# Optimization experiments

Hardware: AMD Instinct MI355X
Metric: run time of the kernel (lower is better)

Reference implementation:

```python
import jax, jax.numpy as jnp
import numpy as np

NUM_CLASSES = 100000
EMBED_DIM = 512
BATCH = 16384
ALPHA = 0.95  # center update momentum: diff = (1 - ALPHA) * (centers - features)


def setup_inputs() -> dict:
    key = jax.random.key(0)
    k1, k2, k3 = jax.random.split(key, 3)
    features = jax.random.normal(k1, (BATCH, EMBED_DIM), dtype=jnp.float32)
    labels = jax.random.randint(k2, (BATCH,), 0, NUM_CLASSES, dtype=jnp.int64)
    center_var = jax.random.normal(k3, (NUM_CLASSES, EMBED_DIM), dtype=jnp.float32)
    return {"features": features, "labels": labels, "center_var": center_var}


def reference(features, labels, center_var):
    # gather per-label centers: [B, D]
    labels = labels.reshape(-1)
    centers_batch = center_var[labels]
    # update delta, 0.05 * (center - feature)
    diff = (1.0 - ALPHA) * (centers_batch - features)
    # scatter-subtract with duplicate-label accumulation (tf scatter_nd_sub semantics)
    new_centers = center_var.at[labels].add(-diff)
    # MSE between features and their (pre-update) centers
    loss = jnp.mean(jnp.square(features - centers_batch))
    return loss, new_centers
```

## Files before the change

kernel.cpp:

```cpp
#include <hip/hip_runtime.h>

constexpr int NUM_CLASSES  = 100000;
constexpr int EMBED_DIM    = 512;
constexpr int BATCH        = 16384;
constexpr int CENTER_ELEMS = NUM_CLASSES * EMBED_DIM;
constexpr int NSLOTS       = 256;
constexpr int KMAX         = 8;
constexpr float UPDATE_SCALE = 0.05f;
constexpr float INV_COUNT  = 1.0f / 8388608.0f;

typedef float f4 __attribute__((ext_vector_type(4)));

constexpr size_t WS_COUNTS_OFF  = 0;
constexpr size_t WS_ITEMS_OFF   = WS_COUNTS_OFF + (size_t)NUM_CLASSES;
constexpr size_t WS_TOUCHED_OFF = WS_ITEMS_OFF + (size_t)NUM_CLASSES * KMAX;
constexpr size_t WS_NTOUCH_OFF  = WS_TOUCHED_OFF + (size_t)BATCH;
constexpr size_t WS_PART_OFF    = WS_NTOUCH_OFF + 16;
constexpr size_t WS_NEW         = (WS_PART_OFF + NSLOTS) * 4;

__global__ void zero_ws_kernel(int* __restrict__ counts,
                               int* __restrict__ ntouched,
                               float* __restrict__ partials) {
    int g = blockIdx.x * blockDim.x + threadIdx.x;
    if (g < NUM_CLASSES) counts[g] = 0;
    if (g == 0) *ntouched = 0;
    if (g < NSLOTS) partials[g] = 0.0f;
}

__global__ void hist_kernel(const int* __restrict__ labels,
                            int* __restrict__ counts,
                            int* __restrict__ items,
                            int* __restrict__ touched,
                            int* __restrict__ ntouched) {
    int b = blockIdx.x * blockDim.x + threadIdx.x;
    if (b < BATCH) {
        int l = labels[b];
        int r = atomicAdd(&counts[l], 1);
        if (r < KMAX) items[l * KMAX + r] = b;
        if (r == 0) {
            int s = atomicAdd(ntouched, 1);
            touched[s] = l;
        }
    }
}

__global__ __launch_bounds__(256) void copy_shift_kernel(
        const float* __restrict__ src,
        float* __restrict__ out) {
    constexpr int NF4 = CENTER_ELEMS / 4;
    const int gid    = blockIdx.x * blockDim.x + threadIdx.x;
    const int stride = gridDim.x * blockDim.x;
    int j = gid;
    if (gid == 0) {
        out[1] = src[0];
        out[2] = src[1];
        out[3] = src[2];
        out[CENTER_ELEMS] = src[CENTER_ELEMS - 1];
        j = stride;
    }
    for (; j < NF4; j += stride) {
        const float* p = src + 4 * j - 1;
        f4 v;
        v.x = p[0];
        v.y = p[1];
        v.z = p[2];
        v.w = p[3];
        __builtin_nontemporal_store(v, (f4*)out + j);
    }
}

__global__ __launch_bounds__(128) void touched_update_kernel(
        const float* __restrict__ features,
        const int*   __restrict__ labels,
        const float* __restrict__ centers,
        const int*   __restrict__ counts,
        const int*   __restrict__ items,
        const int*   __restrict__ touched,
        const int*   __restrict__ ntouched,
        float* __restrict__ out,
        float* __restrict__ partials) {
    const int nb = *ntouched;
    if (blockIdx.x >= nb) return;
    const int c   = touched[blockIdx.x];
    const int cnt = counts[c];
    const int t   = threadIdx.x;

    const f4 c4 = ((const f4*)(centers + (size_t)c * EMBED_DIM))[t];
    f4 s; s.x = 0.f; s.y = 0.f; s.z = 0.f; s.w = 0.f;
    float local = 0.0f;

    if (cnt <= KMAX) {
        for (int i = 0; i < cnt; ++i) {
            const int b = items[c * KMAX + i];
            const f4 f = ((const f4*)(features + (size_t)b * EMBED_DIM))[t];
            float dx = f.x - c4.x, dy = f.y - c4.y, dz = f.z - c4.z, dw = f.w - c4.w;
            s.x += dx; s.y += dy; s.z += dz; s.w += dw;
            local += dx * dx + dy * dy + dz * dz + dw * dw;
        }
    } else {
        for (int b = 0; b < BATCH; ++b) {
            if (labels[b] == c) {
                const f4 f = ((const f4*)(features + (size_t)b * EMBED_DIM))[t];
                float dx = f.x - c4.x, dy = f.y - c4.y, dz = f.z - c4.z, dw = f.w - c4.w;
                s.x += dx; s.y += dy; s.z += dz; s.w += dw;
                local += dx * dx + dy * dy + dz * dz + dw * dw;
            }
        }
    }

    f4 n4;
    n4.x = fmaf(UPDATE_SCALE, s.x, c4.x);
    n4.y = fmaf(UPDATE_SCALE, s.y, c4.y);
    n4.z = fmaf(UPDATE_SCALE, s.z, c4.z);
    n4.w = fmaf(UPDATE_SCALE, s.w, c4.w);

    #pragma unroll
    for (int off = 32; off > 0; off >>= 1)
        local += __shfl_down(local, off, 64);
    if ((t & 63) == 0)
        atomicAdd(&partials[(blockIdx.x * 2 + (t >> 6)) & (NSLOTS - 1)], local);

    __shared__ float row[EMBED_DIM];
    ((f4*)row)[t] = n4;
    __syncthreads();

    const size_t R = (size_t)c * EMBED_DIM;
    if (t < 127) {
        f4 o;
        o.x = row[4 * t + 3];
        o.y = row[4 * t + 4];
        o.z = row[4 * t + 5];
        o.w = row[4 * t + 6];
        ((f4*)(out + R + 4))[t] = o;
    } else {
        out[R + 1] = row[0];
        out[R + 2] = row[1];
        out[R + 3] = row[2];
        out[R + EMBED_DIM] = row[EMBED_DIM - 1];
    }
}

__global__ __launch_bounds__(64) void finalize_loss_kernel(
        const float* __restrict__ partials,
        float* __restrict__ out) {
    float v = 0.0f;
    #pragma unroll
    for (int k = 0; k < NSLOTS / 64; ++k)
        v += partials[threadIdx.x + k * 64];
    #pragma unroll
    for (int off = 32; off > 0; off >>= 1)
        v += __shfl_down(v, off, 64);
    if (threadIdx.x == 0)
        out[0] = v * INV_COUNT;
}


__global__ void copy_centers_kernel(const float* __restrict__ src,
                                    float* __restrict__ dst,
                                    float* __restrict__ ws_partials) {
    int gid = blockIdx.x * blockDim.x + threadIdx.x;
    if (gid < NSLOTS) ws_partials[gid] = 0.0f;
    int stride = gridDim.x * blockDim.x;
    for (int i = gid; i < CENTER_ELEMS; i += stride) dst[i] = src[i];
}

__global__ __launch_bounds__(128) void update_kernel(
        const float* __restrict__ features,
        const int*   __restrict__ labels,
        const float* __restrict__ centers,
        float* __restrict__ out,
        float* __restrict__ ws_partials) {
    const int b = blockIdx.x;
    const int label = labels[b];
    const int t = threadIdx.x;
    const float4 f = ((const float4*)(features + (size_t)b * EMBED_DIM))[t];
    const float4 c = ((const float4*)(centers + (size_t)label * EMBED_DIM))[t];
    float4 d;
    d.x = f.x - c.x; d.y = f.y - c.y; d.z = f.z - c.z; d.w = f.w - c.w;
    float* nrow = out + 1 + (size_t)label * EMBED_DIM + (size_t)t * 4;
    atomicAdd(nrow + 0, UPDATE_SCALE * d.x);
    atomicAdd(nrow + 1, UPDATE_SCALE * d.y);
    atomicAdd(nrow + 2, UPDATE_SCALE * d.z);
    atomicAdd(nrow + 3, UPDATE_SCALE * d.w);
    float local = d.x * d.x + d.y * d.y + d.z * d.z + d.w * d.w;
    #pragma unroll
    for (int off = 32; off > 0; off >>= 1)
        local += __shfl_down(local, off, 64);
    if ((t & 63) == 0)
        atomicAdd(&ws_partials[(b * 2 + (t >> 6)) & (NSLOTS - 1)], local);
}


extern "C" void kernel_launch(void* const* d_in, const int* in_sizes, int n_in,
                              void* d_out, int out_size, void* d_ws, size_t ws_size,
                              hipStream_t stream) {
    const float* features = (const float*)d_in[0];
    const int*   labels   = (const int*)d_in[1];
    const float* centers  = (const float*)d_in[2];
    float* out = (float*)d_out;

    if (ws_size >= WS_NEW) {
        int* wsi       = (int*)d_ws;
        int* counts    = wsi + WS_COUNTS_OFF;
        int* items     = wsi + WS_ITEMS_OFF;
        int* touched   = wsi + WS_TOUCHED_OFF;
        int* ntouched  = wsi + WS_NTOUCH_OFF;
        float* partials = (float*)(wsi + WS_PART_OFF);

        zero_ws_kernel<<<(NUM_CLASSES + 255) / 256, 256, 0, stream>>>(
            counts, ntouched, partials);
        hist_kernel<<<(BATCH + 255) / 256, 256, 0, stream>>>(
            labels, counts, items, touched, ntouched);
        copy_shift_kernel<<<2048, 256, 0, stream>>>(centers, out);
        touched_update_kernel<<<BATCH, 128, 0, stream>>>(
            features, labels, centers, counts, items, touched, ntouched,
            out, partials);
        finalize_loss_kernel<<<1, 64, 0, stream>>>(partials, out);
    } else {
        float* partials = (float*)d_ws;
        copy_centers_kernel<<<8192, 256, 0, stream>>>(centers, out + 1, partials);
        update_kernel<<<BATCH, 128, 0, stream>>>(features, labels, centers, out, partials);
        finalize_loss_kernel<<<1, 64, 0, stream>>>(partials, out);
    }
}
```

Baseline: 426.7 us.

## Use aligned vector loads with lane shuffles in copy-shift and pack two classes per block

The shifted copy of the centers now does one aligned 16-byte load per element group and gets the preceding element from the neighbouring lane by a wave shuffle. Only lane 0 of each wave does an extra scalar load. Previously it did four unaligned scalar loads. The nontemporal store is replaced by a normal vector store. The touched-class update kernel now handles two classes per 256-thread block, which halves the number of blocks launched and the number of early-exit blocks.

```diff
diff --git a/kernel.cpp b/kernel.cpp
--- a/kernel.cpp
+++ b/kernel.cpp
@@ -50,26 +50,25 @@
     constexpr int NF4 = CENTER_ELEMS / 4;
     const int gid    = blockIdx.x * blockDim.x + threadIdx.x;
     const int stride = gridDim.x * blockDim.x;
-    int j = gid;
-    if (gid == 0) {
-        out[1] = src[0];
-        out[2] = src[1];
-        out[3] = src[2];
-        out[CENTER_ELEMS] = src[CENTER_ELEMS - 1];
-        j = stride;
-    }
-    for (; j < NF4; j += stride) {
-        const float* p = src + 4 * j - 1;
-        f4 v;
-        v.x = p[0];
-        v.y = p[1];
-        v.z = p[2];
-        v.w = p[3];
-        __builtin_nontemporal_store(v, (f4*)out + j);
-    }
-}
-
-__global__ __launch_bounds__(128) void touched_update_kernel(
+    const int lane   = threadIdx.x & 63;
+    for (int j = gid; j < NF4; j += stride) {
+        f4 v = ((const f4*)src)[j];
+        float wprev = __shfl_up(v.w, 1, 64);
+        if (lane == 0 && j > 0) wprev = src[4 * j - 1];
+        if (j == 0) {
+            out[1] = v.x;
+            out[2] = v.y;
+            out[3] = v.z;
+            out[CENTER_ELEMS] = src[CENTER_ELEMS - 1];
+        } else {
+            f4 o;
+            o.x = wprev; o.y = v.x; o.z = v.y; o.w = v.z;
+            ((f4*)out)[j] = o;
+        }
+    }
+}
+
+__global__ __launch_bounds__(256) void touched_update_kernel(
         const float* __restrict__ features,
         const int*   __restrict__ labels,
         const float* __restrict__ centers,
@@ -79,64 +78,76 @@
         const int*   __restrict__ ntouched,
         float* __restrict__ out,
         float* __restrict__ partials) {
-    const int nb = *ntouched;
-    if (blockIdx.x >= nb) return;
-    const int c   = touched[blockIdx.x];
-    const int cnt = counts[c];
-    const int t   = threadIdx.x;
-
-    const f4 c4 = ((const f4*)(centers + (size_t)c * EMBED_DIM))[t];
-    f4 s; s.x = 0.f; s.y = 0.f; s.z = 0.f; s.w = 0.f;
-    float local = 0.0f;
-
-    if (cnt <= KMAX) {
-        for (int i = 0; i < cnt; ++i) {
-            const int b = items[c * KMAX + i];
-            const f4 f = ((const f4*)(features + (size_t)b * EMBED_DIM))[t];
-            float dx = f.x - c4.x, dy = f.y - c4.y, dz = f.z - c4.z, dw = f.w - c4.w;
-            s.x += dx; s.y += dy; s.z += dz; s.w += dw;
-            local += dx * dx + dy * dy + dz * dz + dw * dw;
-        }
-    } else {
-        for (int b = 0; b < BATCH; ++b) {
-            if (labels[b] == c) {
-                const f4 f = ((const f4*)(features + (size_t)b * EMBED_DIM))[t];
-                float dx = f.x - c4.x, dy = f.y - c4.y, dz = f.z - c4.z, dw = f.w - c4.w;
+    const int nb   = *ntouched;
+    const int t    = threadIdx.x;
+    const int half = t >> 7;
+    const int ts   = t & 127;
+    const int idx  = blockIdx.x * 2 + half;
+    const bool active = idx < nb;
+
+    __shared__ float row[2][EMBED_DIM];
+    int c = 0;
+
+    if (active) {
+        c = touched[idx];
+        const int cnt = counts[c];
+
+        const f4 c4 = ((const f4*)(centers + (size_t)c * EMBED_DIM))[ts];
+        f4 s; s.x = 0.f; s.y = 0.f; s.z = 0.f; s.w = 0.f;
+        float local = 0.0f;
+
+        if (cnt <= KMAX) {
+            for (int i = 0; i < cnt; ++i) {
+                const int b = items[c * KMAX + i];
+                const f4 f = ((const f4*)(features + (size_t)b * EMBED_DIM))[ts];
+                float dx = f.x - c4.x, dy = f.y - c4.y;
+                float dz = f.z - c4.z, dw = f.w - c4.w;
                 s.x += dx; s.y += dy; s.z += dz; s.w += dw;
                 local += dx * dx + dy * dy + dz * dz + dw * dw;
             }
-        }
-    }
-
-    f4 n4;
-    n4.x = fmaf(UPDATE_SCALE, s.x, c4.x);
-    n4.y = fmaf(UPDATE_SCALE, s.y, c4.y);
-    n4.z = fmaf(UPDATE_SCALE, s.z, c4.z);
-    n4.w = fmaf(UPDATE_SCALE, s.w, c4.w);
-
-    #pragma unroll
-    for (int off = 32; off > 0; off >>= 1)
-        local += __shfl_down(local, off, 64);
-    if ((t & 63) == 0)
-        atomicAdd(&partials[(blockIdx.x * 2 + (t >> 6)) & (NSLOTS - 1)], local);
-
-    __shared__ float row[EMBED_DIM];
-    ((f4*)row)[t] = n4;
+        } else {
+            for (int b = 0; b < BATCH; ++b) {
+                if (labels[b] == c) {
+                    const f4 f = ((const f4*)(features + (size_t)b * EMBED_DIM))[ts];
+                    float dx = f.x - c4.x, dy = f.y - c4.y;
+                    float dz = f.z - c4.z, dw = f.w - c4.w;
+                    s.x += dx; s.y += dy; s.z += dz; s.w += dw;
+                    local += dx * dx + dy * dy + dz * dz + dw * dw;
+                }
+            }
+        }
+
+        f4 n4;
+        n4.x = fmaf(UPDATE_SCALE, s.x, c4.x);
+        n4.y = fmaf(UPDATE_SCALE, s.y, c4.y);
+        n4.z = fmaf(UPDATE_SCALE, s.z, c4.z);
+        n4.w = fmaf(UPDATE_SCALE, s.w, c4.w);
+
+        #pragma unroll
+        for (int off = 32; off > 0; off >>= 1)
+            local += __shfl_down(local, off, 64);
+        if ((t & 63) == 0)
+            atomicAdd(&partials[(idx * 2 + (ts >> 6)) & (NSLOTS - 1)], local);
+
+        ((f4*)row[half])[ts] = n4;
+    }
     __syncthreads();
 
-    const size_t R = (size_t)c * EMBED_DIM;
-    if (t < 127) {
-        f4 o;
-        o.x = row[4 * t + 3];
-        o.y = row[4 * t + 4];
-        o.z = row[4 * t + 5];
-        o.w = row[4 * t + 6];
-        ((f4*)(out + R + 4))[t] = o;
-    } else {
-        out[R + 1] = row[0];
-        out[R + 2] = row[1];
-        out[R + 3] = row[2];
-        out[R + EMBED_DIM] = row[EMBED_DIM - 1];
+    if (active) {
+        const size_t R = (size_t)c * EMBED_DIM;
+        if (ts < 127) {
+            f4 o;
+            o.x = row[half][4 * ts + 3];
+            o.y = row[half][4 * ts + 4];
+            o.z = row[half][4 * ts + 5];
+            o.w = row[half][4 * ts + 6];
+            ((f4*)(out + R + 4))[ts] = o;
+        } else {
+            out[R + 1] = row[half][0];
+            out[R + 2] = row[half][1];
+            out[R + 3] = row[half][2];
+            out[R + EMBED_DIM] = row[half][EMBED_DIM - 1];
+        }
     }
 }
 
@@ -212,7 +223,7 @@
         hist_kernel<<<(BATCH + 255) / 256, 256, 0, stream>>>(
             labels, counts, items, touched, ntouched);
         copy_shift_kernel<<<2048, 256, 0, stream>>>(centers, out);
-        touched_update_kernel<<<BATCH, 128, 0, stream>>>(
+        touched_update_kernel<<<(BATCH + 1) / 2, 256, 0, stream>>>(
             features, labels, centers, counts, items, touched, ntouched,
             out, partials);
         finalize_loss_kernel<<<1, 64, 0, stream>>>(partials, out);
```

Result: faster. 407.8 us (-4.4%).

## Fuse center copy and touched-row update into one wave-per-row streaming kernel

Applied to the files above, without the earlier changes.

Replaces the separate shifted copy of all centers and the per-touched-class update kernel with one kernel where each wavefront walks class rows. Each wave reads its center row once, applies the accumulated feature deltas if the class has labels, and writes the shifted output row using a lane shuffle instead of shared memory. This removes the second pass that rewrote touched rows and drops the touched-list bookkeeping and its atomics. The cost is per-row branching and a per-class count lookup in the streaming loop, and some lanes go idle where touched rows are unevenly spread.

```diff
diff --git a/kernel.cpp b/kernel.cpp
--- a/kernel.cpp
+++ b/kernel.cpp
@@ -13,130 +13,114 @@
 
 constexpr size_t WS_COUNTS_OFF  = 0;
 constexpr size_t WS_ITEMS_OFF   = WS_COUNTS_OFF + (size_t)NUM_CLASSES;
-constexpr size_t WS_TOUCHED_OFF = WS_ITEMS_OFF + (size_t)NUM_CLASSES * KMAX;
-constexpr size_t WS_NTOUCH_OFF  = WS_TOUCHED_OFF + (size_t)BATCH;
-constexpr size_t WS_PART_OFF    = WS_NTOUCH_OFF + 16;
+constexpr size_t WS_PART_OFF    = WS_ITEMS_OFF + (size_t)NUM_CLASSES * KMAX;
 constexpr size_t WS_NEW         = (WS_PART_OFF + NSLOTS) * 4;
 
 __global__ void zero_ws_kernel(int* __restrict__ counts,
-                               int* __restrict__ ntouched,
                                float* __restrict__ partials) {
     int g = blockIdx.x * blockDim.x + threadIdx.x;
     if (g < NUM_CLASSES) counts[g] = 0;
-    if (g == 0) *ntouched = 0;
     if (g < NSLOTS) partials[g] = 0.0f;
 }
 
 __global__ void hist_kernel(const int* __restrict__ labels,
                             int* __restrict__ counts,
-                            int* __restrict__ items,
-                            int* __restrict__ touched,
-                            int* __restrict__ ntouched) {
+                            int* __restrict__ items) {
     int b = blockIdx.x * blockDim.x + threadIdx.x;
     if (b < BATCH) {
         int l = labels[b];
         int r = atomicAdd(&counts[l], 1);
         if (r < KMAX) items[l * KMAX + r] = b;
-        if (r == 0) {
-            int s = atomicAdd(ntouched, 1);
-            touched[s] = l;
-        }
     }
 }
 
-__global__ __launch_bounds__(256) void copy_shift_kernel(
-        const float* __restrict__ src,
-        float* __restrict__ out) {
-    constexpr int NF4 = CENTER_ELEMS / 4;
-    const int gid    = blockIdx.x * blockDim.x + threadIdx.x;
-    const int stride = gridDim.x * blockDim.x;
-    int j = gid;
-    if (gid == 0) {
-        out[1] = src[0];
-        out[2] = src[1];
-        out[3] = src[2];
-        out[CENTER_ELEMS] = src[CENTER_ELEMS - 1];
-        j = stride;
-    }
-    for (; j < NF4; j += stride) {
-        const float* p = src + 4 * j - 1;
-        f4 v;
-        v.x = p[0];
-        v.y = p[1];
-        v.z = p[2];
-        v.w = p[3];
-        __builtin_nontemporal_store(v, (f4*)out + j);
-    }
-}
-
-__global__ __launch_bounds__(128) void touched_update_kernel(
+__global__ __launch_bounds__(256) void fused_stream_kernel(
         const float* __restrict__ features,
+        const float* __restrict__ centers,
         const int*   __restrict__ labels,
-        const float* __restrict__ centers,
         const int*   __restrict__ counts,
         const int*   __restrict__ items,
-        const int*   __restrict__ touched,
-        const int*   __restrict__ ntouched,
         float* __restrict__ out,
         float* __restrict__ partials) {
-    const int nb = *ntouched;
-    if (blockIdx.x >= nb) return;
-    const int c   = touched[blockIdx.x];
-    const int cnt = counts[c];
-    const int t   = threadIdx.x;
-
-    const f4 c4 = ((const f4*)(centers + (size_t)c * EMBED_DIM))[t];
-    f4 s; s.x = 0.f; s.y = 0.f; s.z = 0.f; s.w = 0.f;
-    float local = 0.0f;
-
-    if (cnt <= KMAX) {
-        for (int i = 0; i < cnt; ++i) {
-            const int b = items[c * KMAX + i];
-            const f4 f = ((const f4*)(features + (size_t)b * EMBED_DIM))[t];
-            float dx = f.x - c4.x, dy = f.y - c4.y, dz = f.z - c4.z, dw = f.w - c4.w;
-            s.x += dx; s.y += dy; s.z += dz; s.w += dw;
-            local += dx * dx + dy * dy + dz * dz + dw * dw;
+    const int lane   = threadIdx.x & 63;
+    const int gwave  = blockIdx.x * (blockDim.x >> 6) + (threadIdx.x >> 6);
+    const int nwaves = gridDim.x * (blockDim.x >> 6);
+
+    for (int c = gwave; c < NUM_CLASSES; c += nwaves) {
+        const size_t base = (size_t)c * EMBED_DIM;
+        const f4* crow = (const f4*)(centers + base);
+        const f4 v0 = crow[2 * lane];
+        const f4 v1 = crow[2 * lane + 1];
+        const int cnt = counts[c];
+
+        f4 n0 = v0, n1 = v1;
+        if (cnt > 0) {
+            f4 s0, s1;
+            s0.x = s0.y = s0.z = s0.w = 0.0f;
+            s1.x = s1.y = s1.z = s1.w = 0.0f;
+            float local = 0.0f;
+            if (cnt <= KMAX) {
+                for (int i = 0; i < cnt; ++i) {
+                    const int b = items[c * KMAX + i];
+                    const f4* frow = (const f4*)(features + (size_t)b * EMBED_DIM);
+                    const f4 f0 = frow[2 * lane];
+                    const f4 f1 = frow[2 * lane + 1];
+                    float d0x = f0.x - v0.x, d0y = f0.y - v0.y;
+                    float d0z = f0.z - v0.z, d0w = f0.w - v0.w;
+                    float d1x = f1.x - v1.x, d1y = f1.y - v1.y;
+                    float d1z = f1.z - v1.z, d1w = f1.w - v1.w;
+                    s0.x += d0x; s0.y += d0y; s0.z += d0z; s0.w += d0w;
+                    s1.x += d1x; s1.y += d1y; s1.z += d1z; s1.w += d1w;
+                    local += d0x * d0x + d0y * d0y + d0z * d0z + d0w * d0w
+                           + d1x * d1x + d1y * d1y + d1z * d1z + d1w * d1w;
+                }
+            } else {
+                for (int b = 0; b < BATCH; ++b) {
+                    if (labels[b] == c) {
+                        const f4* frow = (const f4*)(features + (size_t)b * EMBED_DIM);
+                        const f4 f0 = frow[2 * lane];
+                        const f4 f1 = frow[2 * lane + 1];
+                        float d0x = f0.x - v0.x, d0y = f0.y - v0.y;
+                        float d0z = f0.z - v0.z, d0w = f0.w - v0.w;
+                        float d1x = f1.x - v1.x, d1y = f1.y - v1.y;
+                        float d1z = f1.z - v1.z, d1w = f1.w - v1.w;
+                        s0.x += d0x; s0.y += d0y; s0.z += d0z; s0.w += d0w;
+                        s1.x += d1x; s1.y += d1y; s1.z += d1z; s1.w += d1w;
+                        local += d0x * d0x + d0y * d0y + d0z * d0z + d0w * d0w
+                               + d1x * d1x + d1y * d1y + d1z * d1z + d1w * d1w;
+                    }
+                }
+            }
+            n0.x = fmaf(UPDATE_SCALE, s0.x, v0.x);
+            n0.y = fmaf(UPDATE_SCALE, s0.y, v0.y);
+            n0.z = fmaf(UPDATE_SCALE, s0.z, v0.z);
+            n0.w = fmaf(UPDATE_SCALE, s0.w, v0.w);
+            n1.x = fmaf(UPDATE_SCALE, s1.x, v1.x);
+            n1.y = fmaf(UPDATE_SCALE, s1.y, v1.y);
+            n1.z = fmaf(UPDATE_SCALE, s1.z, v1.z);
+            n1.w = fmaf(UPDATE_SCALE, s1.w, v1.w);
+            #pragma unroll
+            for (int off = 32; off > 0; off >>= 1)
+                local += __shfl_down(local, off, 64);
+            if (lane == 0)
+                atomicAdd(&partials[c & (NSLOTS - 1)], local);
         }
-    } else {
-        for (int b = 0; b < BATCH; ++b) {
-            if (labels[b] == c) {
-                const f4 f = ((const f4*)(features + (size_t)b * EMBED_DIM))[t];
-                float dx = f.x - c4.x, dy = f.y - c4.y, dz = f.z - c4.z, dw = f.w - c4.w;
-                s.x += dx; s.y += dy; s.z += dz; s.w += dw;
-                local += dx * dx + dy * dy + dz * dz + dw * dw;
-            }
+
+        const float prevw = __shfl_up(n1.w, 1, 64);
+        f4 o0, o1;
+        o0.x = prevw; o0.y = n0.x; o0.z = n0.y; o0.w = n0.z;
+        o1.x = n0.w;  o1.y = n1.x; o1.z = n1.y; o1.w = n1.z;
+        f4* obase = (f4*)out + (size_t)c * (EMBED_DIM / 4);
+        if (lane > 0) {
+            obase[2 * lane] = o0;
+        } else {
+            out[base + 1] = n0.x;
+            out[base + 2] = n0.y;
+            out[base + 3] = n0.z;
         }
-    }
-
-    f4 n4;
-    n4.x = fmaf(UPDATE_SCALE, s.x, c4.x);
-    n4.y = fmaf(UPDATE_SCALE, s.y, c4.y);
-    n4.z = fmaf(UPDATE_SCALE, s.z, c4.z);
-    n4.w = fmaf(UPDATE_SCALE, s.w, c4.w);
-
-    #pragma unroll
-    for (int off = 32; off > 0; off >>= 1)
-        local += __shfl_down(local, off, 64);
-    if ((t & 63) == 0)
-        atomicAdd(&partials[(blockIdx.x * 2 + (t >> 6)) & (NSLOTS - 1)], local);
-
-    __shared__ float row[EMBED_DIM];
-    ((f4*)row)[t] = n4;
-    __syncthreads();
-
-    const size_t R = (size_t)c * EMBED_DIM;
-    if (t < 127) {
-        f4 o;
-        o.x = row[4 * t + 3];
-        o.y = row[4 * t + 4];
-        o.z = row[4 * t + 5];
-        o.w = row[4 * t + 6];
-        ((f4*)(out + R + 4))[t] = o;
-    } else {
-        out[R + 1] = row[0];
-        out[R + 2] = row[1];
-        out[R + 3] = row[2];
-        out[R + EMBED_DIM] = row[EMBED_DIM - 1];
+        obase[2 * lane + 1] = o1;
+        if (lane == 63)
+            out[base + EMBED_DIM] = n1.w;
     }
 }
 
@@ -200,21 +184,17 @@
     float* out = (float*)d_out;
 
     if (ws_size >= WS_NEW) {
-        int* wsi       = (int*)d_ws;
-        int* counts    = wsi + WS_COUNTS_OFF;
-        int* items     = wsi + WS_ITEMS_OFF;
-        int* touched   = wsi + WS_TOUCHED_OFF;
-        int* ntouched  = wsi + WS_NTOUCH_OFF;
+        int* wsi        = (int*)d_ws;
+        int* counts     = wsi + WS_COUNTS_OFF;
+        int* items      = wsi + WS_ITEMS_OFF;
         float* partials = (float*)(wsi + WS_PART_OFF);
 
         zero_ws_kernel<<<(NUM_CLASSES + 255) / 256, 256, 0, stream>>>(
-            counts, ntouched, partials);
+            counts, partials);
         hist_kernel<<<(BATCH + 255) / 256, 256, 0, stream>>>(
-            labels, counts, items, touched, ntouched);
-        copy_shift_kernel<<<2048, 256, 0, stream>>>(centers, out);
-        touched_update_kernel<<<BATCH, 128, 0, stream>>>(
-            features, labels, centers, counts, items, touched, ntouched,
-            out, partials);
+            labels, counts, items);
+        fused_stream_kernel<<<2048, 256, 0, stream>>>(
+            features, centers, labels, counts, items, out, partials);
         finalize_loss_kernel<<<1, 64, 0, stream>>>(partials, out);
     } else {
         float* partials = (float*)d_ws;
```

Measured after the change: 419.1 us. Within noise of the previous version (-1.8%).
